# Kernel optimization log

Measured on AMD Instinct MI355X. Metric: run time of the kernel, lower is better.

Reference implementation:

```python
import jax, jax.numpy as jnp
import numpy as np

B_, T, I, S, O = 64, 2048, 64, 128, 64

def setup_inputs() -> dict:
    key = jax.random.key(0)
    ks = jax.random.split(key, 7)
    x = jax.random.normal(ks[0], (B_, T, I), dtype=jnp.float32)
    A = jax.random.normal(ks[1], (S, S), dtype=jnp.float32) * 0.1
    Bm = jax.random.normal(ks[2], (S, I), dtype=jnp.float32) * 0.1
    Cm = jax.random.normal(ks[3], (O, S), dtype=jnp.float32) * 0.1
    Dm = jax.random.normal(ks[4], (O, I), dtype=jnp.float32) * 0.1
    W_sel = jax.random.normal(ks[5], (S, I), dtype=jnp.float32) * 0.1
    b_sel = jnp.zeros((S,), jnp.float32)
    ln_gamma = jnp.ones((S,), jnp.float32)
    ln_beta = jnp.zeros((S,), jnp.float32)
    conv_w = jax.random.normal(ks[6], (S, I, 3), dtype=jnp.float32) * 0.1  # Conv1d weight [out,in,k]
    conv_b = jnp.zeros((S,), jnp.float32)
    return {"x": x, "A": A, "B": Bm, "C": Cm, "D": Dm, "W_sel": W_sel,
            "b_sel": b_sel, "ln_gamma": ln_gamma, "ln_beta": ln_beta,
            "conv_w": conv_w, "conv_b": conv_b, "use_parallel": 0}

LN_EPS = 1e-5

def _forward(x, A, B, C, D, W_sel, b_sel, ln_gamma, ln_beta, conv_w, conv_b, use_parallel):
    # x: [B, T, I]
    if use_parallel and x.shape[1] > 10:
        # parallel_scan: conv1d(k=3, pad=1) -> cumsum over time -> project with C
        xc = jnp.transpose(x, (0, 2, 1))  # [B, I, T]
        conv = jax.lax.conv_general_dilated(
            xc, conv_w, window_strides=(1,), padding=((1, 1),),
            dimension_numbers=("NCH", "OIH", "NCH")) + conv_b[None, :, None]
        conv = jnp.transpose(conv, (0, 2, 1))           # [B, T, S]
        out = jnp.cumsum(conv, axis=1) @ C.T            # [B, T, O]
    else:
        # selective_scan: sequential gated SSM with per-step LayerNorm
        def step(h, x_t):
            gate = jax.nn.sigmoid(x_t @ W_sel.T + b_sel)        # [B, S]
            h_new = h @ A.T + x_t @ B.T
            h = gate * h_new + (1.0 - gate) * h
            mu = jnp.mean(h, axis=-1, keepdims=True)
            var = jnp.var(h, axis=-1, keepdims=True)
            h = (h - mu) * jax.lax.rsqrt(var + LN_EPS) * ln_gamma + ln_beta
            y = h @ C.T + x_t @ D.T                              # [B, O]
            return h, y
        h0 = jnp.zeros((x.shape[0], A.shape[0]), x.dtype)
        _, ys = jax.lax.scan(step, h0, jnp.transpose(x, (1, 0, 2)))  # ys: [T, B, O]
        out = jnp.transpose(ys, (1, 0, 2))                           # [B, T, O]
    final = out[:, -1, :]
    diff = jnp.diff(out, axis=1)
    temporal_coherence = 1.0 / (1.0 + jnp.mean(jnp.linalg.norm(diff, axis=-1)))
    state_magnitude = jnp.mean(jnp.linalg.norm(out, axis=-1))
    selection_activity = jnp.mean(jax.nn.sigmoid(jnp.mean(x, axis=1) @ W_sel.T + b_sel))
    state_stability = jnp.mean(jnp.std(out, axis=1, ddof=1))  # torch.std is unbiased
    return final, temporal_coherence, state_magnitude, selection_activity, state_stability

def reference(x, A, B, C, D, W_sel, b_sel, ln_gamma, ln_beta, conv_w, conv_b, use_parallel):
    return _forward(x, A, B, C, D, W_sel, b_sel, ln_gamma, ln_beta, conv_w, conv_b, use_parallel)
```

## Files before the change

### kernel.cpp

```cpp
#include <hip/hip_runtime.h>
#include <math.h>

#define NB 64
#define NT 2048
#define NI 64
#define NS 128
#define NO 64

typedef float4 f4;

#define PIN4(v) asm("" : "+v"((v).x), "+v"((v).y), "+v"((v).z), "+v"((v).w))
#define FMA4(a0,a1,a2,a3,W_,V_) \
    a0 = fmaf((W_).x, (V_).x, a0); a1 = fmaf((W_).y, (V_).y, a1); \
    a2 = fmaf((W_).z, (V_).z, a2); a3 = fmaf((W_).w, (V_).w, a3)

template<int CTRL>
__device__ __forceinline__ float dpp_add(float v) {
    int t = __builtin_amdgcn_update_dpp(0, __float_as_int(v), CTRL, 0xF, 0xF, true);
    return v + __int_as_float(t);
}
__device__ __forceinline__ float qxor1(float v) { return dpp_add<0xB1>(v); }
__device__ __forceinline__ float qxor2(float v) { return dpp_add<0x4E>(v); }
__device__ __forceinline__ float wave_sum63(float v) {
    v = dpp_add<0x111>(v); v = dpp_add<0x112>(v); v = dpp_add<0x114>(v);
// ... 21 lines not shown
    const float* __restrict__ Wsel,
    const float* __restrict__ bsel,
    float* __restrict__ P)
{
    const int b   = blockIdx.x >> 5;
    const int c   = blockIdx.x & 31;
    const int tid = threadIdx.x;

    __shared__ __align__(16) float xs[64][64];
    {
        const f4* src = (const f4*)(x + ((size_t)b * NT + c * 64) * NI);
        f4* dst = (f4*)&xs[0][0];
        #pragma unroll
        for (int k = 0; k < 4; ++k) dst[tid + k * 256] = src[tid + k * 256];
    }

    const float* wrow = (tid < 128) ? (Bm + (size_t)tid * NI)
                                    : (Wsel + (size_t)(tid - 128) * NI);
    const float bias = (tid < 128) ? 0.f : bsel[tid - 128];

    f4 W0,W1,W2,W3,W4,W5,W6,W7,W8,W9,W10,W11,W12,W13,W14,W15;
    {
        const f4* wp = (const f4*)wrow;
        W0=wp[0]; W1=wp[1]; W2=wp[2]; W3=wp[3]; W4=wp[4]; W5=wp[5]; W6=wp[6]; W7=wp[7];
        W8=wp[8]; W9=wp[9]; W10=wp[10]; W11=wp[11]; W12=wp[12]; W13=wp[13]; W14=wp[14]; W15=wp[15];
    }
    PIN4(W0); PIN4(W1); PIN4(W2); PIN4(W3); PIN4(W4); PIN4(W5); PIN4(W6); PIN4(W7);
    PIN4(W8); PIN4(W9); PIN4(W10); PIN4(W11); PIN4(W12); PIN4(W13); PIN4(W14); PIN4(W15);

    __syncthreads();

// ... 11 lines not shown
        v = xr[6];  FMA4(a0,a1,a2,a3,W6,v);
        v = xr[7];  FMA4(a0,a1,a2,a3,W7,v);
        v = xr[8];  FMA4(a0,a1,a2,a3,W8,v);
        v = xr[9];  FMA4(a0,a1,a2,a3,W9,v);
        v = xr[10]; FMA4(a0,a1,a2,a3,W10,v);
        v = xr[11]; FMA4(a0,a1,a2,a3,W11,v);
        v = xr[12]; FMA4(a0,a1,a2,a3,W12,v);
        v = xr[13]; FMA4(a0,a1,a2,a3,W13,v);
        v = xr[14]; FMA4(a0,a1,a2,a3,W14,v);
        v = xr[15]; FMA4(a0,a1,a2,a3,W15,v);
        pout[(size_t)t * 256] = (a0 + a1) + (a2 + a3);
    }
}

template<int USEP>
__global__ __launch_bounds__(512, 2) void scan_kernel(
    const float* __restrict__ x,
    const float* __restrict__ P,
    const float* __restrict__ A,
    const float* __restrict__ Bm,
    const float* __restrict__ Wsel,
    const float* __restrict__ bsel,
    const float* __restrict__ gamma,
    const float* __restrict__ beta,
    float* __restrict__ H,
    float* __restrict__ musig)
{
    const int b    = blockIdx.x;
    const int tid  = threadIdx.x;
    const int q    = tid & 3;
    const int r    = tid >> 2;
    const int lane = tid & 63;
    const int wave = tid >> 6;

    __shared__ __align__(16) float hbuf[2][148];
    __shared__ __align__(16) float red[2][16];
    __shared__ __align__(16) float plds[2][32][USEP ? 256 : 64];

    f4 Aw0, Aw1, Aw2, Aw3, Aw4, Aw5, Aw6, Aw7;
    float sAg = 0.f, aB = 0.f;
    {
        const f4* ga = (const f4*)(gamma + q * 32);
        const f4* bb = (const f4*)(beta  + q * 32);
        const f4* Ap = (const f4*)(A + (size_t)r * NS + q * 32);
        f4 g, be_, v;
#define LOADA(J, AW) \
        g = ga[J]; be_ = bb[J]; v = Ap[J]; \
        AW.x = v.x * g.x; AW.y = v.y * g.y; AW.z = v.z * g.z; AW.w = v.w * g.w; \
        sAg += (AW.x + AW.y) + (AW.z + AW.w); \
        aB = fmaf(v.x, be_.x, aB); aB = fmaf(v.y, be_.y, aB); \
        aB = fmaf(v.z, be_.z, aB); aB = fmaf(v.w, be_.w, aB);
        LOADA(0, Aw0) LOADA(1, Aw1) LOADA(2, Aw2) LOADA(3, Aw3)
        LOADA(4, Aw4) LOADA(5, Aw5) LOADA(6, Aw6) LOADA(7, Aw7)
#undef LOADA
        sAg = qxor2(qxor1(sAg));
        aB  = qxor2(qxor1(aB));
    }
    PIN4(Aw0); PIN4(Aw1); PIN4(Aw2); PIN4(Aw3);
    PIN4(Aw4); PIN4(Aw5); PIN4(Aw6); PIN4(Aw7);

    f4 Bw0, Bw1, Bw2, Bw3, Ww0, Ww1, Ww2, Ww3;
    float bs = 0.f;
    if constexpr (!USEP) {
        const f4* Bp = (const f4*)(Bm   + (size_t)r * NI + q * 16);
        const f4* Wp = (const f4*)(Wsel + (size_t)r * NI + q * 16);
        Bw0 = Bp[0]; Bw1 = Bp[1]; Bw2 = Bp[2]; Bw3 = Bp[3];
        Ww0 = Wp[0]; Ww1 = Wp[1]; Ww2 = Wp[2]; Ww3 = Wp[3];
        bs = bsel[r];
        PIN4(Bw0); PIN4(Bw1); PIN4(Bw2); PIN4(Bw3);
        PIN4(Ww0); PIN4(Ww1); PIN4(Ww2); PIN4(Ww3);
        asm("" : "+v"(bs));
    }
    float gm = gamma[r], bt = beta[r];
    asm("" : "+v"(sAg), "+v"(aB), "+v"(gm), "+v"(bt));

    const float* xstage = x + (size_t)b * NT * NI + wave * 256 + lane * 4;
    const float* pstage = P + (size_t)b * NT * 256 + wave * 256 + lane * 4;
    if constexpr (USEP) {
        #pragma unroll
        for (int c = 0; c < 2; ++c)
            #pragma unroll
            for (int k = 0; k < 4; ++k)
                stage16(pstage + (size_t)(c * 32 + k * 8) * 256,
                        &plds[c][k * 8 + wave][0]);
    } else {
        stage16(xstage,        &plds[0][wave * 4][0]);
        stage16(xstage + 2048, &plds[1][wave * 4][0]);
    }
    asm volatile("s_waitcnt vmcnt(0)" ::: "memory");
    __syncthreads();

    float zp = 0.f, dBp = 0.f;
    float pbp = 0.f, pzp = 0.f;
    auto xdots = [&](int t) {
        const f4* xp = (const f4*)&plds[(t >> 5) & 1][t & 31][q * 16];
        f4 v0 = xp[0], v1 = xp[1], v2 = xp[2], v3 = xp[3];
        float p0 = 0.f, p1 = 0.f, p2 = 0.f, p3 = 0.f;
        float w0 = 0.f, w1 = 0.f, w2 = 0.f, w3 = 0.f;
        FMA4(p0, p1, p2, p3, Bw0, v0); FMA4(p0, p1, p2, p3, Bw1, v1);
        FMA4(p0, p1, p2, p3, Bw2, v2); FMA4(p0, p1, p2, p3, Bw3, v3);
        FMA4(w0, w1, w2, w3, Ww0, v0); FMA4(w0, w1, w2, w3, Ww1, v1);
        FMA4(w0, w1, w2, w3, Ww2, v2); FMA4(w0, w1, w2, w3, Ww3, v3);
        dBp = qxor2(qxor1((p0 + p1) + (p2 + p3)));
        zp  = qxor2(qxor1((w0 + w1) + (w2 + w3))) + bs;
    };
    auto pread = [&](int t) {
        const float* pl = &plds[(t >> 5) & 1][t & 31][0];
        pbp = pl[r]; pzp = pl[128 + r];
    };

    float*  Hb   = H + ((size_t)b * NT) * NS;
    float2* musb = (float2*)musig + (size_t)b * NT;

    float mp;
    if constexpr (USEP) pread(0); else xdots(0);
    {
        float g = sigmoidf_fast(USEP ? pzp : zp);
        mp = g * (USEP ? pbp : dBp);
        if (q == 0) {
            hbuf[0][((r >> 5) * 36) + (r & 31)] = mp;
            Hb[r] = mp;
        }
        float s  = wave_sum63(mp);
        float s2 = wave_sum63(mp * mp);
        if (lane == 63) { red[0][wave] = s; red[0][8 + wave] = s2; }
    }
    if constexpr (USEP) pread(1); else xdots(1);
    bar_lds();

    auto body = [&](int t, int parIn, int parOut) {
        const f4* rp = (const f4*)&red[parIn][0];
        f4 sa = rp[0], sb = rp[1], sc = rp[2], sd = rp[3];
        float S  = ((sa.x + sa.y) + (sa.z + sa.w)) + ((sb.x + sb.y) + (sb.z + sb.w));
        float S2 = ((sc.x + sc.y) + (sc.z + sc.w)) + ((sd.x + sd.y) + (sd.z + sd.w));
        float mu   = S * (1.0f / 512.0f);
        float var  = fmaf(S2, 1.0f / 512.0f, -mu * mu);
        float rstd = 1.0f / sqrtf(var + 1e-5f);
        const f4* hp = (const f4*)&hbuf[parIn][q * 36];
        f4 h0 = hp[0], h1 = hp[1], h2 = hp[2], h3 = hp[3];
        f4 h4 = hp[4], h5 = hp[5], h6 = hp[6], h7 = hp[7];
        float d0 = 0.f, d1 = 0.f, d2 = 0.f, d3 = 0.f;
        FMA4(d0, d1, d2, d3, Aw0, h0); FMA4(d0, d1, d2, d3, Aw1, h1);
        FMA4(d0, d1, d2, d3, Aw2, h2); FMA4(d0, d1, d2, d3, Aw3, h3);
        FMA4(d0, d1, d2, d3, Aw4, h4); FMA4(d0, d1, d2, d3, Aw5, h5);
        FMA4(d0, d1, d2, d3, Aw6, h6); FMA4(d0, d1, d2, d3, Aw7, h7);
        float dAm = qxor2(qxor1((d0 + d1) + (d2 + d3)));
        float dA  = fmaf(rstd, fmaf(-mu, sAg, dAm), aB);
        float hpl = fmaf((mp - mu) * rstd, gm, bt);
        float g   = sigmoidf_fast(USEP ? pzp : zp);
        float hn  = dA + (USEP ? pbp : dBp);
        float m   = fmaf(g, hn - hpl, hpl);
        if (q == 0) {
            hbuf[parOut][((r >> 5) * 36) + (r & 31)] = m;
            Hb[(size_t)t * NS + r] = m;
        }
        float s  = wave_sum63(m);
        float s2 = wave_sum63(m * m);
        if (lane == 63) { red[parOut][wave] = s; red[parOut][8 + wave] = s2; }
        if (tid == 0) musb[t - 1] = make_float2(mu, rstd);
        mp = m;
        if (t + 1 < NT) { if constexpr (USEP) pread(t + 1); else xdots(t + 1); }
        bar_lds();
    };

    auto boundary = [&](int t) {
        const int s2 = (t >> 5) + 2;
        if constexpr (USEP) {
            if (s2 < NT / 32) {
                #pragma unroll
                for (int k = 0; k < 4; ++k)
                    stage16(pstage + (size_t)(s2 * 32 + k * 8) * 256,
                            &plds[s2 & 1][k * 8 + wave][0]);
            }
            asm volatile("s_waitcnt vmcnt(4)" ::: "memory");
        } else {
            if (s2 < NT / 32)
                stage16(xstage + (size_t)s2 * 2048, &plds[s2 & 1][wave * 4][0]);
            asm volatile("s_waitcnt vmcnt(1)" ::: "memory");
        }
        __builtin_amdgcn_s_barrier();
        asm volatile("" ::: "memory");
    };

    for (int t = 1; t + 1 < NT; t += 2) {
        body(t, 0, 1);
        body(t + 1, 1, 0);
        if (((t + 1) & 31) == 30) boundary(t + 1);
    }
    body(NT - 1, 0, 1);

    {
        const f4* rp = (const f4*)&red[1][0];
        f4 sa = rp[0], sb = rp[1], sc = rp[2], sd = rp[3];
        float S  = ((sa.x + sa.y) + (sa.z + sa.w)) + ((sb.x + sb.y) + (sb.z + sb.w));
        float S2 = ((sc.x + sc.y) + (sc.z + sc.w)) + ((sd.x + sd.y) + (sd.z + sd.w));
        float mu   = S * (1.0f / 512.0f);
        float var  = fmaf(S2, 1.0f / 512.0f, -mu * mu);
        float rstd = 1.0f / sqrtf(var + 1e-5f);
        if (tid == 0) musb[NT - 1] = make_float2(mu, rstd);
    }
}

#define CHUNKS 32
#define TCH (NT / CHUNKS)

__global__ __launch_bounds__(512, 1) void y_stats_kernel(
    const float* __restrict__ H,
    const float* __restrict__ x,
    const float* __restrict__ Cm,
    const float* __restrict__ Dm,
    const float* __restrict__ gamma,
    const float* __restrict__ beta,
    const float* __restrict__ musig,
    float* __restrict__ SY,
    float* __restrict__ SYY,
    float* __restrict__ meanx,
    float* __restrict__ nsum,
    float* __restrict__ dsum,
    float* __restrict__ outFinal)
{
    const int b     = blockIdx.x >> 5;
    const int chunk = blockIdx.x & 31;
    const int tid   = threadIdx.x;
    const int o2    = tid & 31;
    const int kq    = (tid >> 5) & 3;
    const int tg    = tid >> 7;
    const int lane  = tid & 63;
    const int sub   = tid >> 6;
    const int o     = tid & 63;

    __shared__ float pbuf[TCH + 1][2 * NO];
    __shared__ float nd[2];

    f4 CA0,CA1,CA2,CA3,CA4,CA5,CA6,CA7, CB0,CB1,CB2,CB3,CB4,CB5,CB6,CB7;
    float sCgA = 0.f, cBA = 0.f, sCgB = 0.f, cBB = 0.f;
    {
        const f4* cpA = (const f4*)(Cm + (size_t)o2 * NS + kq * 32);
        const f4* cpB = (const f4*)(Cm + (size_t)(o2 + 32) * NS + kq * 32);
        const f4* gp  = (const f4*)(gamma + kq * 32);
        const f4* bp  = (const f4*)(beta  + kq * 32);
        f4 vv, gg, bb;
#define LC(J, CW, CP, SG, CBs) \
        vv = CP[J]; gg = gp[J]; bb = bp[J]; \
        CW.x = vv.x * gg.x; CW.y = vv.y * gg.y; CW.z = vv.z * gg.z; CW.w = vv.w * gg.w; \
        SG += (CW.x + CW.y) + (CW.z + CW.w); \
        CBs = fmaf(vv.x, bb.x, CBs); CBs = fmaf(vv.y, bb.y, CBs); \
        CBs = fmaf(vv.z, bb.z, CBs); CBs = fmaf(vv.w, bb.w, CBs);
        LC(0,CA0,cpA,sCgA,cBA) LC(1,CA1,cpA,sCgA,cBA) LC(2,CA2,cpA,sCgA,cBA) LC(3,CA3,cpA,sCgA,cBA)
        LC(4,CA4,cpA,sCgA,cBA) LC(5,CA5,cpA,sCgA,cBA) LC(6,CA6,cpA,sCgA,cBA) LC(7,CA7,cpA,sCgA,cBA)
        LC(0,CB0,cpB,sCgB,cBB) LC(1,CB1,cpB,sCgB,cBB) LC(2,CB2,cpB,sCgB,cBB) LC(3,CB3,cpB,sCgB,cBB)
        LC(4,CB4,cpB,sCgB,cBB) LC(5,CB5,cpB,sCgB,cBB) LC(6,CB6,cpB,sCgB,cBB) LC(7,CB7,cpB,sCgB,cBB)
#undef LC
    }
    f4 DA0,DA1,DA2,DA3, DB0,DB1,DB2,DB3;
    {
        const f4* dpA = (const f4*)(Dm + (size_t)o2 * NI + kq * 16);
        const f4* dpB = (const f4*)(Dm + (size_t)(o2 + 32) * NI + kq * 16);
        DA0 = dpA[0]; DA1 = dpA[1]; DA2 = dpA[2]; DA3 = dpA[3];
        DB0 = dpB[0]; DB1 = dpB[1]; DB2 = dpB[2]; DB3 = dpB[3];
    }
    PIN4(CA0); PIN4(CA1); PIN4(CA2); PIN4(CA3); PIN4(CA4); PIN4(CA5); PIN4(CA6); PIN4(CA7);
    PIN4(CB0); PIN4(CB1); PIN4(CB2); PIN4(CB3); PIN4(CB4); PIN4(CB5); PIN4(CB6); PIN4(CB7);
    PIN4(DA0); PIN4(DA1); PIN4(DA2); PIN4(DA3); PIN4(DB0); PIN4(DB1); PIN4(DB2); PIN4(DB3);
    asm("" : "+v"(sCgA), "+v"(cBA), "+v"(sCgB), "+v"(cBB));

    const float*  Hb  = H + ((size_t)b * NT) * NS;
    const float*  xb  = x + ((size_t)b * NT) * NI;
    const float2* msb = (const float2*)musig + (size_t)b * NT;
    const int t0 = chunk * TCH;

    if (tid < 2) nd[tid] = 0.f;

    if (sub < 4) {
        float s = 0.f;
        const float* xk = xb + o;
        #pragma unroll 4
        for (int i = 0; i < 16; ++i) s += xk[(size_t)(t0 + sub * 16 + i) * NI];
        atomicAdd(&meanx[b * NI + o], s);
    }

    {
        const int khigh = sub & 1;
        const int i_start = (tg == 0 && t0 > 0) ? -1 : 0;
        for (int i = i_start; i < 16; ++i) {
            const int t = t0 + tg * 16 + i;
            float2 ms = msb[t];
            const f4* hp = (const f4*)(Hb + (size_t)t * NS + kq * 32);
            const f4* xp = (const f4*)(xb + (size_t)t * NI + kq * 16);
            float a0=0.f,a1=0.f,a2=0.f,a3=0.f, b0=0.f,b1=0.f,b2=0.f,b3=0.f;
            f4 hv;
            hv = hp[0]; FMA4(a0,a1,a2,a3,CA0,hv); FMA4(b0,b1,b2,b3,CB0,hv);
            hv = hp[1]; FMA4(a0,a1,a2,a3,CA1,hv); FMA4(b0,b1,b2,b3,CB1,hv);
            hv = hp[2]; FMA4(a0,a1,a2,a3,CA2,hv); FMA4(b0,b1,b2,b3,CB2,hv);
            hv = hp[3]; FMA4(a0,a1,a2,a3,CA3,hv); FMA4(b0,b1,b2,b3,CB3,hv);
            hv = hp[4]; FMA4(a0,a1,a2,a3,CA4,hv); FMA4(b0,b1,b2,b3,CB4,hv);
            hv = hp[5]; FMA4(a0,a1,a2,a3,CA5,hv); FMA4(b0,b1,b2,b3,CB5,hv);
            hv = hp[6]; FMA4(a0,a1,a2,a3,CA6,hv); FMA4(b0,b1,b2,b3,CB6,hv);
            hv = hp[7]; FMA4(a0,a1,a2,a3,CA7,hv); FMA4(b0,b1,b2,b3,CB7,hv);
            float hdotA = (a0 + a1) + (a2 + a3);
            float hdotB = (b0 + b1) + (b2 + b3);
            float xa0=0.f,xa1=0.f,xa2=0.f,xa3=0.f, xb0=0.f,xb1=0.f,xb2=0.f,xb3=0.f;
            hv = xp[0]; FMA4(xa0,xa1,xa2,xa3,DA0,hv); FMA4(xb0,xb1,xb2,xb3,DB0,hv);
            hv = xp[1]; FMA4(xa0,xa1,xa2,xa3,DA1,hv); FMA4(xb0,xb1,xb2,xb3,DB1,hv);
            hv = xp[2]; FMA4(xa0,xa1,xa2,xa3,DA2,hv); FMA4(xb0,xb1,xb2,xb3,DB2,hv);
            hv = xp[3]; FMA4(xa0,xa1,xa2,xa3,DA3,hv); FMA4(xb0,xb1,xb2,xb3,DB3,hv);
            float xdotA = (xa0 + xa1) + (xa2 + xa3);
            float xdotB = (xb0 + xb1) + (xb2 + xb3);
            float pa = fmaf(ms.y, fmaf(-ms.x, sCgA, hdotA), cBA + xdotA);
            float pb = fmaf(ms.y, fmaf(-ms.x, sCgB, hdotB), cBB + xdotB);
            pa += __shfl_xor(pa, 32);
            pb += __shfl_xor(pb, 32);
            const int row = tg * 16 + i + 1;
            const int col = khigh * 64 + o2 + ((lane >= 32) ? 32 : 0);
            pbuf[row][col] = (lane >= 32) ? pb : pa;
        }
    }
    __syncthreads();

    {
        const int tt0 = sub * 8;
        float yprev = pbuf[tt0][o] + pbuf[tt0][64 + o];
        float sy = 0.f, syy = 0.f, na = 0.f, da = 0.f;
        #pragma unroll
        for (int ii = 0; ii < 8; ++ii) {
            const int row = tt0 + ii + 1;
            float y = pbuf[row][o] + pbuf[row][64 + o];
            sy  += y;
            syy += y * y;
            float n2 = wave_sum63(y * y);
            na += sqrtf(n2);
            if (t0 + tt0 + ii > 0) {
                float df = y - yprev;
                float d2 = wave_sum63(df * df);
                da += sqrtf(d2);
            }
            yprev = y;
            if (chunk == 31 && sub == 7 && ii == 7)
                outFinal[b * NO + o] = y;
        }
        atomicAdd(&SY[b * NO + o], sy);
        atomicAdd(&SYY[b * NO + o], syy);
        if (lane == 63) {
            atomicAdd(&nd[0], na);
            atomicAdd(&nd[1], da);
        }
    }
    __syncthreads();
    if (tid == 0) { atomicAdd(nsum, nd[0]); atomicAdd(dsum, nd[1]); }
}

__global__ __launch_bounds__(256) void finalize_kernel(
    const float* __restrict__ Wsel,
    const float* __restrict__ bsel,
    const float* __restrict__ meanx,
    const float* __restrict__ SY,
    const float* __restrict__ SYY,
    const float* __restrict__ nsum,
    const float* __restrict__ dsum,
    float* __restrict__ out)
{
    const int tid  = threadIdx.x;
    const int wave = tid >> 6;
    const int lane = tid & 63;
// ... 46 lines not shown
    const float* Bm    = (const float*)d_in[2];
    const float* Cm    = (const float*)d_in[3];
    const float* Dm    = (const float*)d_in[4];
    const float* Wsel  = (const float*)d_in[5];
    const float* bsel  = (const float*)d_in[6];
    const float* gamma = (const float*)d_in[7];
    const float* beta  = (const float*)d_in[8];
    float* out = (float*)d_out;

    char* ws = (char*)d_ws;
    float* SY    = (float*)(ws + 0);
    float* SYY   = (float*)(ws + 16384);
    float* meanx = (float*)(ws + 32768);
    float* nsum  = (float*)(ws + 49152);
    float* dsum  = (float*)(ws + 49156);
    const size_t zbytes = 49160;

    const size_t offH  = 65536;
    float* H     = (float*)(ws + offH);
    const size_t offMu = offH + (size_t)NB * NT * NS * sizeof(float);
    float* musig = (float*)(ws + offMu);
    const size_t offP  = offMu + (size_t)NB * NT * 2 * sizeof(float);
    float* P     = (float*)(ws + offP);
    const size_t needP = offP + (size_t)NB * NT * 256 * sizeof(float);

    const bool useP = (ws_size >= needP);

    hipMemsetAsync(ws, 0, zbytes, stream);
    if (useP) {
        proj_kernel<<<NB * 32, 256, 0, stream>>>(x, Bm, Wsel, bsel, P);
        scan_kernel<1><<<NB, 512, 0, stream>>>(x, P, A, Bm, Wsel, bsel,
                                               gamma, beta, H, musig);
    } else {
        scan_kernel<0><<<NB, 512, 0, stream>>>(x, (const float*)ws, A, Bm, Wsel,
                                               bsel, gamma, beta, H, musig);
    }
    y_stats_kernel<<<NB * CHUNKS, 512, 0, stream>>>(H, x, Cm, Dm, gamma, beta, musig,
                                                    SY, SYY, meanx, nsum, dsum, out);
    finalize_kernel<<<1, 256, 0, stream>>>(Wsel, bsel, meanx, SY, SYY, nsum, dsum, out);
}
```

Baseline: 1.681 ms.

## Fuse scan and output-stats kernels with producer-consumer progress flags

Merges the sequential scan kernel and the y-statistics kernel into one persistent launch. The first NB blocks run the per-batch scan and publish progress every 64 steps through release atomics. The remaining blocks act as consumers that spin on those flags and process 64-step chunks, so the output projection overlaps the scan instead of running after it. This relies on all blocks being co-resident and adds spin-wait and fence overhead, with fewer consumer blocks than the old separate grid.

Result: slower. 2.540 ms (+51.1%).

```diff
diff --git a/kernel.cpp b/kernel.cpp
--- a/kernel.cpp
+++ b/kernel.cpp
@@ -6,6 +6,8 @@
 #define NI 64
 #define NS 128
 #define NO 64
+
+#define LDS_BYTES 83968
 
 typedef float4 f4;
 
@@ -59,7 +61,6 @@
         #pragma unroll
         for (int k = 0; k < 4; ++k) dst[tid + k * 256] = src[tid + k * 256];
     }
-
     const float* wrow = (tid < 128) ? (Bm + (size_t)tid * NI)
                                     : (Wsel + (size_t)(tid - 128) * NI);
     const float bias = (tid < 128) ? 0.f : bsel[tid - 128];
@@ -101,7 +102,7 @@
 }
 
 template<int USEP>
-__global__ __launch_bounds__(512, 2) void scan_kernel(
+__global__ __launch_bounds__(512, 1) void fused_kernel(
     const float* __restrict__ x,
     const float* __restrict__ P,
     const float* __restrict__ A,
@@ -110,330 +111,350 @@
     const float* __restrict__ bsel,
     const float* __restrict__ gamma,
     const float* __restrict__ beta,
-    float* __restrict__ H,
-    float* __restrict__ musig)
-{
-    const int b    = blockIdx.x;
-    const int tid  = threadIdx.x;
-    const int q    = tid & 3;
-    const int r    = tid >> 2;
-    const int lane = tid & 63;
-    const int wave = tid >> 6;
-
-    __shared__ __align__(16) float hbuf[2][148];
-    __shared__ __align__(16) float red[2][16];
-    __shared__ __align__(16) float plds[2][32][USEP ? 256 : 64];
-
-    f4 Aw0, Aw1, Aw2, Aw3, Aw4, Aw5, Aw6, Aw7;
-    float sAg = 0.f, aB = 0.f;
-    {
-        const f4* ga = (const f4*)(gamma + q * 32);
-        const f4* bb = (const f4*)(beta  + q * 32);
-        const f4* Ap = (const f4*)(A + (size_t)r * NS + q * 32);
-        f4 g, be_, v;
-#define LOADA(J, AW) \
-        g = ga[J]; be_ = bb[J]; v = Ap[J]; \
-        AW.x = v.x * g.x; AW.y = v.y * g.y; AW.z = v.z * g.z; AW.w = v.w * g.w; \
-        sAg += (AW.x + AW.y) + (AW.z + AW.w); \
-        aB = fmaf(v.x, be_.x, aB); aB = fmaf(v.y, be_.y, aB); \
-        aB = fmaf(v.z, be_.z, aB); aB = fmaf(v.w, be_.w, aB);
-        LOADA(0, Aw0) LOADA(1, Aw1) LOADA(2, Aw2) LOADA(3, Aw3)
-        LOADA(4, Aw4) LOADA(5, Aw5) LOADA(6, Aw6) LOADA(7, Aw7)
-#undef LOADA
-        sAg = qxor2(qxor1(sAg));
-        aB  = qxor2(qxor1(aB));
-    }
-    PIN4(Aw0); PIN4(Aw1); PIN4(Aw2); PIN4(Aw3);
-    PIN4(Aw4); PIN4(Aw5); PIN4(Aw6); PIN4(Aw7);
-
-    f4 Bw0, Bw1, Bw2, Bw3, Ww0, Ww1, Ww2, Ww3;
-    float bs = 0.f;
-    if constexpr (!USEP) {
-        const f4* Bp = (const f4*)(Bm   + (size_t)r * NI + q * 16);
-        const f4* Wp = (const f4*)(Wsel + (size_t)r * NI + q * 16);
-        Bw0 = Bp[0]; Bw1 = Bp[1]; Bw2 = Bp[2]; Bw3 = Bp[3];
-        Ww0 = Wp[0]; Ww1 = Wp[1]; Ww2 = Wp[2]; Ww3 = Wp[3];
-        bs = bsel[r];
-        PIN4(Bw0); PIN4(Bw1); PIN4(Bw2); PIN4(Bw3);
-        PIN4(Ww0); PIN4(Ww1); PIN4(Ww2); PIN4(Ww3);
-        asm("" : "+v"(bs));
-    }
-    float gm = gamma[r], bt = beta[r];
-    asm("" : "+v"(sAg), "+v"(aB), "+v"(gm), "+v"(bt));
-
-    const float* xstage = x + (size_t)b * NT * NI + wave * 256 + lane * 4;
-    const float* pstage = P + (size_t)b * NT * 256 + wave * 256 + lane * 4;
-    if constexpr (USEP) {
-        #pragma unroll
-        for (int c = 0; c < 2; ++c)
-            #pragma unroll
-            for (int k = 0; k < 4; ++k)
-                stage16(pstage + (size_t)(c * 32 + k * 8) * 256,
-                        &plds[c][k * 8 + wave][0]);
-    } else {
-        stage16(xstage,        &plds[0][wave * 4][0]);
-        stage16(xstage + 2048, &plds[1][wave * 4][0]);
-    }
-    asm volatile("s_waitcnt vmcnt(0)" ::: "memory");
-    __syncthreads();
-
-    float zp = 0.f, dBp = 0.f;
-    float pbp = 0.f, pzp = 0.f;
-    auto xdots = [&](int t) {
-        const f4* xp = (const f4*)&plds[(t >> 5) & 1][t & 31][q * 16];
-        f4 v0 = xp[0], v1 = xp[1], v2 = xp[2], v3 = xp[3];
-        float p0 = 0.f, p1 = 0.f, p2 = 0.f, p3 = 0.f;
-        float w0 = 0.f, w1 = 0.f, w2 = 0.f, w3 = 0.f;
-        FMA4(p0, p1, p2, p3, Bw0, v0); FMA4(p0, p1, p2, p3, Bw1, v1);
-        FMA4(p0, p1, p2, p3, Bw2, v2); FMA4(p0, p1, p2, p3, Bw3, v3);
-        FMA4(w0, w1, w2, w3, Ww0, v0); FMA4(w0, w1, w2, w3, Ww1, v1);
-        FMA4(w0, w1, w2, w3, Ww2, v2); FMA4(w0, w1, w2, w3, Ww3, v3);
-        dBp = qxor2(qxor1((p0 + p1) + (p2 + p3)));
-        zp  = qxor2(qxor1((w0 + w1) + (w2 + w3))) + bs;
-    };
-    auto pread = [&](int t) {
-        const float* pl = &plds[(t >> 5) & 1][t & 31][0];
-        pbp = pl[r]; pzp = pl[128 + r];
-    };
-
-    float*  Hb   = H + ((size_t)b * NT) * NS;
-    float2* musb = (float2*)musig + (size_t)b * NT;
-
-    float mp;
-    if constexpr (USEP) pread(0); else xdots(0);
-    {
-        float g = sigmoidf_fast(USEP ? pzp : zp);
-        mp = g * (USEP ? pbp : dBp);
-        if (q == 0) {
-            hbuf[0][((r >> 5) * 36) + (r & 31)] = mp;
-            Hb[r] = mp;
-        }
-        float s  = wave_sum63(mp);
-        float s2 = wave_sum63(mp * mp);
-        if (lane == 63) { red[0][wave] = s; red[0][8 + wave] = s2; }
-    }
-    if constexpr (USEP) pread(1); else xdots(1);
-    bar_lds();
-
-    auto body = [&](int t, int parIn, int parOut) {
-        const f4* rp = (const f4*)&red[parIn][0];
-        f4 sa = rp[0], sb = rp[1], sc = rp[2], sd = rp[3];
-        float S  = ((sa.x + sa.y) + (sa.z + sa.w)) + ((sb.x + sb.y) + (sb.z + sb.w));
-        float S2 = ((sc.x + sc.y) + (sc.z + sc.w)) + ((sd.x + sd.y) + (sd.z + sd.w));
-        float mu   = S * (1.0f / 512.0f);
-        float var  = fmaf(S2, 1.0f / 512.0f, -mu * mu);
-        float rstd = 1.0f / sqrtf(var + 1e-5f);
-        const f4* hp = (const f4*)&hbuf[parIn][q * 36];
-        f4 h0 = hp[0], h1 = hp[1], h2 = hp[2], h3 = hp[3];
-        f4 h4 = hp[4], h5 = hp[5], h6 = hp[6], h7 = hp[7];
-        float d0 = 0.f, d1 = 0.f, d2 = 0.f, d3 = 0.f;
-        FMA4(d0, d1, d2, d3, Aw0, h0); FMA4(d0, d1, d2, d3, Aw1, h1);
-        FMA4(d0, d1, d2, d3, Aw2, h2); FMA4(d0, d1, d2, d3, Aw3, h3);
-        FMA4(d0, d1, d2, d3, Aw4, h4); FMA4(d0, d1, d2, d3, Aw5, h5);
-        FMA4(d0, d1, d2, d3, Aw6, h6); FMA4(d0, d1, d2, d3, Aw7, h7);
-        float dAm = qxor2(qxor1((d0 + d1) + (d2 + d3)));
-        float dA  = fmaf(rstd, fmaf(-mu, sAg, dAm), aB);
-        float hpl = fmaf((mp - mu) * rstd, gm, bt);
-        float g   = sigmoidf_fast(USEP ? pzp : zp);
-        float hn  = dA + (USEP ? pbp : dBp);
-        float m   = fmaf(g, hn - hpl, hpl);
-        if (q == 0) {
-            hbuf[parOut][((r >> 5) * 36) + (r & 31)] = m;
-            Hb[(size_t)t * NS + r] = m;
-        }
-        float s  = wave_sum63(m);
-        float s2 = wave_sum63(m * m);
-        if (lane == 63) { red[parOut][wave] = s; red[parOut][8 + wave] = s2; }
-        if (tid == 0) musb[t - 1] = make_float2(mu, rstd);
-        mp = m;
-        if (t + 1 < NT) { if constexpr (USEP) pread(t + 1); else xdots(t + 1); }
-        bar_lds();
-    };
-
-    auto boundary = [&](int t) {
-        const int s2 = (t >> 5) + 2;
-        if constexpr (USEP) {
-            if (s2 < NT / 32) {
-                #pragma unroll
-                for (int k = 0; k < 4; ++k)
-                    stage16(pstage + (size_t)(s2 * 32 + k * 8) * 256,
-                            &plds[s2 & 1][k * 8 + wave][0]);
-            }
-            asm volatile("s_waitcnt vmcnt(4)" ::: "memory");
-        } else {
-            if (s2 < NT / 32)
-                stage16(xstage + (size_t)s2 * 2048, &plds[s2 & 1][wave * 4][0]);
-            asm volatile("s_waitcnt vmcnt(1)" ::: "memory");
-        }
-        __builtin_amdgcn_s_barrier();
-        asm volatile("" ::: "memory");
-    };
-
-    for (int t = 1; t + 1 < NT; t += 2) {
-        body(t, 0, 1);
-        body(t + 1, 1, 0);
-        if (((t + 1) & 31) == 30) boundary(t + 1);
-    }
-    body(NT - 1, 0, 1);
-
-    {
-        const f4* rp = (const f4*)&red[1][0];
-        f4 sa = rp[0], sb = rp[1], sc = rp[2], sd = rp[3];
-        float S  = ((sa.x + sa.y) + (sa.z + sa.w)) + ((sb.x + sb.y) + (sb.z + sb.w));
-        float S2 = ((sc.x + sc.y) + (sc.z + sc.w)) + ((sd.x + sd.y) + (sd.z + sd.w));
-        float mu   = S * (1.0f / 512.0f);
-        float var  = fmaf(S2, 1.0f / 512.0f, -mu * mu);
-        float rstd = 1.0f / sqrtf(var + 1e-5f);
-        if (tid == 0) musb[NT - 1] = make_float2(mu, rstd);
-    }
-}
-
-#define CHUNKS 32
-#define TCH (NT / CHUNKS)
-
-__global__ __launch_bounds__(512, 1) void y_stats_kernel(
-    const float* __restrict__ H,
-    const float* __restrict__ x,
     const float* __restrict__ Cm,
     const float* __restrict__ Dm,
-    const float* __restrict__ gamma,
-    const float* __restrict__ beta,
-    const float* __restrict__ musig,
+    float* __restrict__ H,
+    float* __restrict__ musig,
     float* __restrict__ SY,
     float* __restrict__ SYY,
     float* __restrict__ meanx,
     float* __restrict__ nsum,
     float* __restrict__ dsum,
-    float* __restrict__ outFinal)
+    int*   __restrict__ progress,
+    float* __restrict__ outFinal,
+    int nCons)
 {
-    const int b     = blockIdx.x >> 5;
-    const int chunk = blockIdx.x & 31;
-    const int tid   = threadIdx.x;
-    const int o2    = tid & 31;
-    const int kq    = (tid >> 5) & 3;
-    const int tg    = tid >> 7;
-    const int lane  = tid & 63;
-    const int sub   = tid >> 6;
-    const int o     = tid & 63;
-
-    __shared__ float pbuf[TCH + 1][2 * NO];
-    __shared__ float nd[2];
-
-    f4 CA0,CA1,CA2,CA3,CA4,CA5,CA6,CA7, CB0,CB1,CB2,CB3,CB4,CB5,CB6,CB7;
-    float sCgA = 0.f, cBA = 0.f, sCgB = 0.f, cBB = 0.f;
+    __shared__ __align__(16) char raw[LDS_BYTES];
+    const int blk = blockIdx.x;
+    const int tid = threadIdx.x;
+    const int lane = tid & 63;
+    const int wave = tid >> 6;
+
+    if (blk < NB) {
+        const int b = blk;
+        const int q = tid & 3;
+        const int r = tid >> 2;
+        constexpr int PW = USEP ? 256 : 64;
+
+        float* hb   = (float*)raw;
+        float* rd   = (float*)(raw + 1184);
+        float* plds = (float*)(raw + 1312);
+
+        f4 Aw0, Aw1, Aw2, Aw3, Aw4, Aw5, Aw6, Aw7;
+        float sAg = 0.f, aB = 0.f;
+        {
+            const f4* ga = (const f4*)(gamma + q * 32);
+            const f4* bb = (const f4*)(beta  + q * 32);
+            const f4* Ap = (const f4*)(A + (size_t)r * NS + q * 32);
+            f4 g, be_, v;
+#define LOADA(J, AW) \
+            g = ga[J]; be_ = bb[J]; v = Ap[J]; \
+            AW.x = v.x * g.x; AW.y = v.y * g.y; AW.z = v.z * g.z; AW.w = v.w * g.w; \
+            sAg += (AW.x + AW.y) + (AW.z + AW.w); \
+            aB = fmaf(v.x, be_.x, aB); aB = fmaf(v.y, be_.y, aB); \
+            aB = fmaf(v.z, be_.z, aB); aB = fmaf(v.w, be_.w, aB);
+            LOADA(0, Aw0) LOADA(1, Aw1) LOADA(2, Aw2) LOADA(3, Aw3)
+            LOADA(4, Aw4) LOADA(5, Aw5) LOADA(6, Aw6) LOADA(7, Aw7)
+#undef LOADA
+            sAg = qxor2(qxor1(sAg));
+            aB  = qxor2(qxor1(aB));
+        }
+        PIN4(Aw0); PIN4(Aw1); PIN4(Aw2); PIN4(Aw3);
+        PIN4(Aw4); PIN4(Aw5); PIN4(Aw6); PIN4(Aw7);
+
+        f4 Bw0, Bw1, Bw2, Bw3, Ww0, Ww1, Ww2, Ww3;
+        float bs = 0.f;
+        if constexpr (!USEP) {
+            const f4* Bp = (const f4*)(Bm   + (size_t)r * NI + q * 16);
+            const f4* Wp = (const f4*)(Wsel + (size_t)r * NI + q * 16);
+            Bw0 = Bp[0]; Bw1 = Bp[1]; Bw2 = Bp[2]; Bw3 = Bp[3];
+            Ww0 = Wp[0]; Ww1 = Wp[1]; Ww2 = Wp[2]; Ww3 = Wp[3];
+            bs = bsel[r];
+            PIN4(Bw0); PIN4(Bw1); PIN4(Bw2); PIN4(Bw3);
+            PIN4(Ww0); PIN4(Ww1); PIN4(Ww2); PIN4(Ww3);
+            asm("" : "+v"(bs));
+        }
+        float gm = gamma[r], bt = beta[r];
+        asm("" : "+v"(sAg), "+v"(aB), "+v"(gm), "+v"(bt));
+
+        const float* xstage = x + (size_t)b * NT * NI + wave * 256 + lane * 4;
+        const float* pstage = P + (size_t)b * NT * 256 + wave * 256 + lane * 4;
+        if constexpr (USEP) {
+            #pragma unroll
+            for (int c = 0; c < 2; ++c)
+                #pragma unroll
+                for (int k = 0; k < 4; ++k)
+                    stage16(pstage + (size_t)(c * 32 + k * 8) * 256,
+                            plds + (c * 32 + k * 8 + wave) * PW);
+        } else {
+            stage16(xstage,        plds + (0 * 32 + wave * 4) * PW);
+            stage16(xstage + 2048, plds + (1 * 32 + wave * 4) * PW);
+        }
+        asm volatile("s_waitcnt vmcnt(0)" ::: "memory");
+        __syncthreads();
+
+        float zp = 0.f, dBp = 0.f, pbp = 0.f, pzp = 0.f;
+        auto xdots = [&](int t) {
+            const f4* xp = (const f4*)(plds + (((t >> 5) & 1) * 32 + (t & 31)) * PW + q * 16);
+            f4 v0 = xp[0], v1 = xp[1], v2 = xp[2], v3 = xp[3];
+            float p0 = 0.f, p1 = 0.f, p2 = 0.f, p3 = 0.f;
+            float w0 = 0.f, w1 = 0.f, w2 = 0.f, w3 = 0.f;
+            FMA4(p0, p1, p2, p3, Bw0, v0); FMA4(p0, p1, p2, p3, Bw1, v1);
+            FMA4(p0, p1, p2, p3, Bw2, v2); FMA4(p0, p1, p2, p3, Bw3, v3);
+            FMA4(w0, w1, w2, w3, Ww0, v0); FMA4(w0, w1, w2, w3, Ww1, v1);
+            FMA4(w0, w1, w2, w3, Ww2, v2); FMA4(w0, w1, w2, w3, Ww3, v3);
+            dBp = qxor2(qxor1((p0 + p1) + (p2 + p3)));
+            zp  = qxor2(qxor1((w0 + w1) + (w2 + w3))) + bs;
+        };
+        auto pread = [&](int t) {
+            const float* pl = plds + (((t >> 5) & 1) * 32 + (t & 31)) * PW;
+            pbp = pl[r]; pzp = pl[128 + r];
+        };
+
+        float*  Hb   = H + ((size_t)b * NT) * NS;
+        float2* musb = (float2*)musig + (size_t)b * NT;
+
+        float mp;
+        if constexpr (USEP) pread(0); else xdots(0);
+        {
+            float g = sigmoidf_fast(USEP ? pzp : zp);
+            mp = g * (USEP ? pbp : dBp);
+            if (q == 0) {
+                hb[0 * 148 + ((r >> 5) * 36) + (r & 31)] = mp;
+                Hb[r] = mp;
+            }
+            float s  = wave_sum63(mp);
+            float s2 = wave_sum63(mp * mp);
+            if (lane == 63) { rd[wave] = s; rd[8 + wave] = s2; }
+        }
+        if constexpr (USEP) pread(1); else xdots(1);
+        bar_lds();
+
+        auto body = [&](int t, int parIn, int parOut) {
+            const f4* rp = (const f4*)(rd + parIn * 16);
+            f4 sa = rp[0], sb = rp[1], sc = rp[2], sd = rp[3];
+            float S  = ((sa.x + sa.y) + (sa.z + sa.w)) + ((sb.x + sb.y) + (sb.z + sb.w));
+            float S2 = ((sc.x + sc.y) + (sc.z + sc.w)) + ((sd.x + sd.y) + (sd.z + sd.w));
+            float mu   = S * (1.0f / 512.0f);
+            float var  = fmaf(S2, 1.0f / 512.0f, -mu * mu);
+            float rstd = 1.0f / sqrtf(var + 1e-5f);
+            const f4* hp = (const f4*)(hb + parIn * 148 + q * 36);
+            f4 h0 = hp[0], h1 = hp[1], h2 = hp[2], h3 = hp[3];
+            f4 h4 = hp[4], h5 = hp[5], h6 = hp[6], h7 = hp[7];
+            float d0 = 0.f, d1 = 0.f, d2 = 0.f, d3 = 0.f;
+            FMA4(d0, d1, d2, d3, Aw0, h0); FMA4(d0, d1, d2, d3, Aw1, h1);
+            FMA4(d0, d1, d2, d3, Aw2, h2); FMA4(d0, d1, d2, d3, Aw3, h3);
+            FMA4(d0, d1, d2, d3, Aw4, h4); FMA4(d0, d1, d2, d3, Aw5, h5);
+            FMA4(d0, d1, d2, d3, Aw6, h6); FMA4(d0, d1, d2, d3, Aw7, h7);
+            float dAm = qxor2(qxor1((d0 + d1) + (d2 + d3)));
+            float dA  = fmaf(rstd, fmaf(-mu, sAg, dAm), aB);
+            float hpl = fmaf((mp - mu) * rstd, gm, bt);
+            float g   = sigmoidf_fast(USEP ? pzp : zp);
+            float hn  = dA + (USEP ? pbp : dBp);
+            float m   = fmaf(g, hn - hpl, hpl);
+            if (q == 0) {
+                hb[parOut * 148 + ((r >> 5) * 36) + (r & 31)] = m;
+                Hb[(size_t)t * NS + r] = m;
+            }
+            float s  = wave_sum63(m);
+            float s2 = wave_sum63(m * m);
+            if (lane == 63) { rd[parOut * 16 + wave] = s; rd[parOut * 16 + 8 + wave] = s2; }
+            if (tid == 0) musb[t - 1] = make_float2(mu, rstd);
+            mp = m;
+            if (t + 1 < NT) { if constexpr (USEP) pread(t + 1); else xdots(t + 1); }
+            bar_lds();
+        };
+
+        auto boundary = [&](int t) {
+            const int s2 = (t >> 5) + 2;
+            if constexpr (USEP) {
+                if (s2 < NT / 32) {
+                    #pragma unroll
+                    for (int k = 0; k < 4; ++k)
+                        stage16(pstage + (size_t)(s2 * 32 + k * 8) * 256,
+                                plds + ((s2 & 1) * 32 + k * 8 + wave) * PW);
+                }
+                asm volatile("s_waitcnt vmcnt(4)" ::: "memory");
+            } else {
+                if (s2 < NT / 32)
+                    stage16(xstage + (size_t)s2 * 2048, plds + ((s2 & 1) * 32 + wave * 4) * PW);
+                asm volatile("s_waitcnt vmcnt(1)" ::: "memory");
+            }
+            __builtin_amdgcn_s_barrier();
+            asm volatile("" ::: "memory");
+        };
+
+        for (int t = 1; t + 1 < NT; t += 2) {
+            body(t, 0, 1);
+            body(t + 1, 1, 0);
+            if (((t + 1) & 31) == 30) boundary(t + 1);
+            if (((t + 1) & 63) == 0) {
+                __threadfence();
+                __builtin_amdgcn_s_barrier();
+                if (tid == 0)
+                    __hip_atomic_store(&progress[b], (t + 1) >> 6,
+                                       __ATOMIC_RELEASE, __HIP_MEMORY_SCOPE_AGENT);
+            }
+        }
+        body(NT - 1, 0, 1);
+        {
+            const f4* rp = (const f4*)(rd + 1 * 16);
+            f4 sa = rp[0], sb = rp[1], sc = rp[2], sd = rp[3];
+            float S  = ((sa.x + sa.y) + (sa.z + sa.w)) + ((sb.x + sb.y) + (sb.z + sb.w));
+            float S2 = ((sc.x + sc.y) + (sc.z + sc.w)) + ((sd.x + sd.y) + (sd.z + sd.w));
+            float mu   = S * (1.0f / 512.0f);
+            float var  = fmaf(S2, 1.0f / 512.0f, -mu * mu);
+            float rstd = 1.0f / sqrtf(var + 1e-5f);
+            if (tid == 0) musb[NT - 1] = make_float2(mu, rstd);
+        }
+        __threadfence();
+        __builtin_amdgcn_s_barrier();
+        if (tid == 0)
+            __hip_atomic_store(&progress[b], 32,
+                               __ATOMIC_RELEASE, __HIP_MEMORY_SCOPE_AGENT);
+        return;
+    }
+
     {
-        const f4* cpA = (const f4*)(Cm + (size_t)o2 * NS + kq * 32);
-        const f4* cpB = (const f4*)(Cm + (size_t)(o2 + 32) * NS + kq * 32);
-        const f4* gp  = (const f4*)(gamma + kq * 32);
-        const f4* bp  = (const f4*)(beta  + kq * 32);
-        f4 vv, gg, bb;
+        const int k    = blk - NB;
+        const int o2   = tid & 31;
+        const int kq   = (tid >> 5) & 3;
+        const int tg   = tid >> 7;
+        const int sub  = tid >> 6;
+        const int o    = tid & 63;
+
+        float (*pbuf)[128] = (float(*)[128])raw;
+        float* nd = (float*)(raw + 65 * 128 * 4);
+
+        f4 CA0,CA1,CA2,CA3,CA4,CA5,CA6,CA7, CB0,CB1,CB2,CB3,CB4,CB5,CB6,CB7;
+        float sCgA = 0.f, cBA = 0.f, sCgB = 0.f, cBB = 0.f;
+        {
+            const f4* cpA = (const f4*)(Cm + (size_t)o2 * NS + kq * 32);
+            const f4* cpB = (const f4*)(Cm + (size_t)(o2 + 32) * NS + kq * 32);
+            const f4* gp  = (const f4*)(gamma + kq * 32);
+            const f4* bp  = (const f4*)(beta  + kq * 32);
+            f4 vv, gg, bb;
 #define LC(J, CW, CP, SG, CBs) \
-        vv = CP[J]; gg = gp[J]; bb = bp[J]; \
-        CW.x = vv.x * gg.x; CW.y = vv.y * gg.y; CW.z = vv.z * gg.z; CW.w = vv.w * gg.w; \
-        SG += (CW.x + CW.y) + (CW.z + CW.w); \
-        CBs = fmaf(vv.x, bb.x, CBs); CBs = fmaf(vv.y, bb.y, CBs); \
-        CBs = fmaf(vv.z, bb.z, CBs); CBs = fmaf(vv.w, bb.w, CBs);
-        LC(0,CA0,cpA,sCgA,cBA) LC(1,CA1,cpA,sCgA,cBA) LC(2,CA2,cpA,sCgA,cBA) LC(3,CA3,cpA,sCgA,cBA)
-        LC(4,CA4,cpA,sCgA,cBA) LC(5,CA5,cpA,sCgA,cBA) LC(6,CA6,cpA,sCgA,cBA) LC(7,CA7,cpA,sCgA,cBA)
-        LC(0,CB0,cpB,sCgB,cBB) LC(1,CB1,cpB,sCgB,cBB) LC(2,CB2,cpB,sCgB,cBB) LC(3,CB3,cpB,sCgB,cBB)
-        LC(4,CB4,cpB,sCgB,cBB) LC(5,CB5,cpB,sCgB,cBB) LC(6,CB6,cpB,sCgB,cBB) LC(7,CB7,cpB,sCgB,cBB)
+            vv = CP[J]; gg = gp[J]; bb = bp[J]; \
+            CW.x = vv.x * gg.x; CW.y = vv.y * gg.y; CW.z = vv.z * gg.z; CW.w = vv.w * gg.w; \
+            SG += (CW.x + CW.y) + (CW.z + CW.w); \
+            CBs = fmaf(vv.x, bb.x, CBs); CBs = fmaf(vv.y, bb.y, CBs); \
+            CBs = fmaf(vv.z, bb.z, CBs); CBs = fmaf(vv.w, bb.w, CBs);
+            LC(0,CA0,cpA,sCgA,cBA) LC(1,CA1,cpA,sCgA,cBA) LC(2,CA2,cpA,sCgA,cBA) LC(3,CA3,cpA,sCgA,cBA)
+            LC(4,CA4,cpA,sCgA,cBA) LC(5,CA5,cpA,sCgA,cBA) LC(6,CA6,cpA,sCgA,cBA) LC(7,CA7,cpA,sCgA,cBA)
+            LC(0,CB0,cpB,sCgB,cBB) LC(1,CB1,cpB,sCgB,cBB) LC(2,CB2,cpB,sCgB,cBB) LC(3,CB3,cpB,sCgB,cBB)
+            LC(4,CB4,cpB,sCgB,cBB) LC(5,CB5,cpB,sCgB,cBB) LC(6,CB6,cpB,sCgB,cBB) LC(7,CB7,cpB,sCgB,cBB)
 #undef LC
-    }
-    f4 DA0,DA1,DA2,DA3, DB0,DB1,DB2,DB3;
-    {
-        const f4* dpA = (const f4*)(Dm + (size_t)o2 * NI + kq * 16);
-        const f4* dpB = (const f4*)(Dm + (size_t)(o2 + 32) * NI + kq * 16);
-        DA0 = dpA[0]; DA1 = dpA[1]; DA2 = dpA[2]; DA3 = dpA[3];
-        DB0 = dpB[0]; DB1 = dpB[1]; DB2 = dpB[2]; DB3 = dpB[3];
-    }
-    PIN4(CA0); PIN4(CA1); PIN4(CA2); PIN4(CA3); PIN4(CA4); PIN4(CA5); PIN4(CA6); PIN4(CA7);
-    PIN4(CB0); PIN4(CB1); PIN4(CB2); PIN4(CB3); PIN4(CB4); PIN4(CB5); PIN4(CB6); PIN4(CB7);
-    PIN4(DA0); PIN4(DA1); PIN4(DA2); PIN4(DA3); PIN4(DB0); PIN4(DB1); PIN4(DB2); PIN4(DB3);
-    asm("" : "+v"(sCgA), "+v"(cBA), "+v"(sCgB), "+v"(cBB));
-
-    const float*  Hb  = H + ((size_t)b * NT) * NS;
-    const float*  xb  = x + ((size_t)b * NT) * NI;
-    const float2* msb = (const float2*)musig + (size_t)b * NT;
-    const int t0 = chunk * TCH;
-
-    if (tid < 2) nd[tid] = 0.f;
-
-    if (sub < 4) {
-        float s = 0.f;
-        const float* xk = xb + o;
-        #pragma unroll 4
-        for (int i = 0; i < 16; ++i) s += xk[(size_t)(t0 + sub * 16 + i) * NI];
-        atomicAdd(&meanx[b * NI + o], s);
-    }
-
-    {
-        const int khigh = sub & 1;
-        const int i_start = (tg == 0 && t0 > 0) ? -1 : 0;
-        for (int i = i_start; i < 16; ++i) {
-            const int t = t0 + tg * 16 + i;
-            float2 ms = msb[t];
-            const f4* hp = (const f4*)(Hb + (size_t)t * NS + kq * 32);
-            const f4* xp = (const f4*)(xb + (size_t)t * NI + kq * 16);
-            float a0=0.f,a1=0.f,a2=0.f,a3=0.f, b0=0.f,b1=0.f,b2=0.f,b3=0.f;
-            f4 hv;
-            hv = hp[0]; FMA4(a0,a1,a2,a3,CA0,hv); FMA4(b0,b1,b2,b3,CB0,hv);
-            hv = hp[1]; FMA4(a0,a1,a2,a3,CA1,hv); FMA4(b0,b1,b2,b3,CB1,hv);
-            hv = hp[2]; FMA4(a0,a1,a2,a3,CA2,hv); FMA4(b0,b1,b2,b3,CB2,hv);
-            hv = hp[3]; FMA4(a0,a1,a2,a3,CA3,hv); FMA4(b0,b1,b2,b3,CB3,hv);
-            hv = hp[4]; FMA4(a0,a1,a2,a3,CA4,hv); FMA4(b0,b1,b2,b3,CB4,hv);
-            hv = hp[5]; FMA4(a0,a1,a2,a3,CA5,hv); FMA4(b0,b1,b2,b3,CB5,hv);
-            hv = hp[6]; FMA4(a0,a1,a2,a3,CA6,hv); FMA4(b0,b1,b2,b3,CB6,hv);
-            hv = hp[7]; FMA4(a0,a1,a2,a3,CA7,hv); FMA4(b0,b1,b2,b3,CB7,hv);
-            float hdotA = (a0 + a1) + (a2 + a3);
-            float hdotB = (b0 + b1) + (b2 + b3);
-            float xa0=0.f,xa1=0.f,xa2=0.f,xa3=0.f, xb0=0.f,xb1=0.f,xb2=0.f,xb3=0.f;
-            hv = xp[0]; FMA4(xa0,xa1,xa2,xa3,DA0,hv); FMA4(xb0,xb1,xb2,xb3,DB0,hv);
-            hv = xp[1]; FMA4(xa0,xa1,xa2,xa3,DA1,hv); FMA4(xb0,xb1,xb2,xb3,DB1,hv);
-            hv = xp[2]; FMA4(xa0,xa1,xa2,xa3,DA2,hv); FMA4(xb0,xb1,xb2,xb3,DB2,hv);
-            hv = xp[3]; FMA4(xa0,xa1,xa2,xa3,DA3,hv); FMA4(xb0,xb1,xb2,xb3,DB3,hv);
-            float xdotA = (xa0 + xa1) + (xa2 + xa3);
-            float xdotB = (xb0 + xb1) + (xb2 + xb3);
-            float pa = fmaf(ms.y, fmaf(-ms.x, sCgA, hdotA), cBA + xdotA);
-            float pb = fmaf(ms.y, fmaf(-ms.x, sCgB, hdotB), cBB + xdotB);
-            pa += __shfl_xor(pa, 32);
-            pb += __shfl_xor(pb, 32);
-            const int row = tg * 16 + i + 1;
-            const int col = khigh * 64 + o2 + ((lane >= 32) ? 32 : 0);
-            pbuf[row][col] = (lane >= 32) ? pb : pa;
-        }
-    }
-    __syncthreads();
-
-    {
-        const int tt0 = sub * 8;
-        float yprev = pbuf[tt0][o] + pbuf[tt0][64 + o];
-        float sy = 0.f, syy = 0.f, na = 0.f, da = 0.f;
-        #pragma unroll
-        for (int ii = 0; ii < 8; ++ii) {
-            const int row = tt0 + ii + 1;
-            float y = pbuf[row][o] + pbuf[row][64 + o];
-            sy  += y;
-            syy += y * y;
-            float n2 = wave_sum63(y * y);
-            na += sqrtf(n2);
-            if (t0 + tt0 + ii > 0) {
-                float df = y - yprev;
-                float d2 = wave_sum63(df * df);
-                da += sqrtf(d2);
-            }
-            yprev = y;
-            if (chunk == 31 && sub == 7 && ii == 7)
-                outFinal[b * NO + o] = y;
-        }
-        atomicAdd(&SY[b * NO + o], sy);
-        atomicAdd(&SYY[b * NO + o], syy);
-        if (lane == 63) {
-            atomicAdd(&nd[0], na);
-            atomicAdd(&nd[1], da);
-        }
-    }
-    __syncthreads();
-    if (tid == 0) { atomicAdd(nsum, nd[0]); atomicAdd(dsum, nd[1]); }
+        }
+        f4 DA0,DA1,DA2,DA3, DB0,DB1,DB2,DB3;
+        {
+            const f4* dpA = (const f4*)(Dm + (size_t)o2 * NI + kq * 16);
+            const f4* dpB = (const f4*)(Dm + (size_t)(o2 + 32) * NI + kq * 16);
+            DA0 = dpA[0]; DA1 = dpA[1]; DA2 = dpA[2]; DA3 = dpA[3];
+            DB0 = dpB[0]; DB1 = dpB[1]; DB2 = dpB[2]; DB3 = dpB[3];
+        }
+        PIN4(CA0); PIN4(CA1); PIN4(CA2); PIN4(CA3); PIN4(CA4); PIN4(CA5); PIN4(CA6); PIN4(CA7);
+        PIN4(CB0); PIN4(CB1); PIN4(CB2); PIN4(CB3); PIN4(CB4); PIN4(CB5); PIN4(CB6); PIN4(CB7);
+        PIN4(DA0); PIN4(DA1); PIN4(DA2); PIN4(DA3); PIN4(DB0); PIN4(DB1); PIN4(DB2); PIN4(DB3);
+        asm("" : "+v"(sCgA), "+v"(cBA), "+v"(sCgB), "+v"(cBB));
+
+        if (tid < 2) nd[tid] = 0.f;
+        __syncthreads();
+
+        for (int u = k; u < NB * 32; u += nCons) {
+            const int c  = u >> 6;
+            const int bb = u & 63;
+            const float*  Hb  = H + ((size_t)bb * NT) * NS;
+            const float*  xb  = x + ((size_t)bb * NT) * NI;
+            const float2* msb = (const float2*)musig + (size_t)bb * NT;
+            const int t0 = c * 64;
+
+            if (sub < 4) {
+                float s = 0.f;
+                const float* xk = xb + o;
+                #pragma unroll 4
+                for (int i = 0; i < 16; ++i) s += xk[(size_t)(t0 + sub * 16 + i) * NI];
+                atomicAdd(&meanx[bb * NI + o], s);
+            }
+
+            if (tid == 0) {
+                while (__hip_atomic_load(&progress[bb], __ATOMIC_ACQUIRE,
+                                         __HIP_MEMORY_SCOPE_AGENT) <= c)
+                    __builtin_amdgcn_s_sleep(16);
+            }
+            __syncthreads();
+
+            {
+                const int khigh = sub & 1;
+                const int i_start = (tg == 0 && t0 > 0) ? -1 : 0;
+                for (int i = i_start; i < 16; ++i) {
+                    const int t = t0 + tg * 16 + i;
+                    float2 ms = msb[t];
+                    const f4* hp = (const f4*)(Hb + (size_t)t * NS + kq * 32);
+                    const f4* xp = (const f4*)(xb + (size_t)t * NI + kq * 16);
+                    float a0=0.f,a1=0.f,a2=0.f,a3=0.f, b0=0.f,b1=0.f,b2=0.f,b3=0.f;
+                    f4 hv;
+                    hv = hp[0]; FMA4(a0,a1,a2,a3,CA0,hv); FMA4(b0,b1,b2,b3,CB0,hv);
+                    hv = hp[1]; FMA4(a0,a1,a2,a3,CA1,hv); FMA4(b0,b1,b2,b3,CB1,hv);
+                    hv = hp[2]; FMA4(a0,a1,a2,a3,CA2,hv); FMA4(b0,b1,b2,b3,CB2,hv);
+                    hv = hp[3]; FMA4(a0,a1,a2,a3,CA3,hv); FMA4(b0,b1,b2,b3,CB3,hv);
+                    hv = hp[4]; FMA4(a0,a1,a2,a3,CA4,hv); FMA4(b0,b1,b2,b3,CB4,hv);
+                    hv = hp[5]; FMA4(a0,a1,a2,a3,CA5,hv); FMA4(b0,b1,b2,b3,CB5,hv);
+                    hv = hp[6]; FMA4(a0,a1,a2,a3,CA6,hv); FMA4(b0,b1,b2,b3,CB6,hv);
+                    hv = hp[7]; FMA4(a0,a1,a2,a3,CA7,hv); FMA4(b0,b1,b2,b3,CB7,hv);
+                    float hdotA = (a0 + a1) + (a2 + a3);
+                    float hdotB = (b0 + b1) + (b2 + b3);
+                    float xa0=0.f,xa1=0.f,xa2=0.f,xa3=0.f, xb0=0.f,xb1=0.f,xb2=0.f,xb3=0.f;
+                    hv = xp[0]; FMA4(xa0,xa1,xa2,xa3,DA0,hv); FMA4(xb0,xb1,xb2,xb3,DB0,hv);
+                    hv = xp[1]; FMA4(xa0,xa1,xa2,xa3,DA1,hv); FMA4(xb0,xb1,xb2,xb3,DB1,hv);
+                    hv = xp[2]; FMA4(xa0,xa1,xa2,xa3,DA2,hv); FMA4(xb0,xb1,xb2,xb3,DB2,hv);
+                    hv = xp[3]; FMA4(xa0,xa1,xa2,xa3,DA3,hv); FMA4(xb0,xb1,xb2,xb3,DB3,hv);
+                    float xdotA = (xa0 + xa1) + (xa2 + xa3);
+                    float xdotB = (xb0 + xb1) + (xb2 + xb3);
+                    float pa = fmaf(ms.y, fmaf(-ms.x, sCgA, hdotA), cBA + xdotA);
+                    float pb = fmaf(ms.y, fmaf(-ms.x, sCgB, hdotB), cBB + xdotB);
+                    pa += __shfl_xor(pa, 32);
+                    pb += __shfl_xor(pb, 32);
+                    const int row = tg * 16 + i + 1;
+                    const int col = khigh * 64 + o2 + ((lane >= 32) ? 32 : 0);
+                    pbuf[row][col] = (lane >= 32) ? pb : pa;
+                }
+            }
+            __syncthreads();
+
+            {
+                const int tt0 = sub * 8;
+                float yprev = pbuf[tt0][o] + pbuf[tt0][64 + o];
+                float sy = 0.f, syy = 0.f, na = 0.f, da = 0.f;
+                #pragma unroll
+                for (int ii = 0; ii < 8; ++ii) {
+                    const int row = tt0 + ii + 1;
+                    float y = pbuf[row][o] + pbuf[row][64 + o];
+                    sy  += y;
+                    syy += y * y;
+                    float n2 = wave_sum63(y * y);
+                    na += sqrtf(n2);
+                    if (t0 + tt0 + ii > 0) {
+                        float df = y - yprev;
+                        float d2 = wave_sum63(df * df);
+                        da += sqrtf(d2);
+                    }
+                    yprev = y;
+                    if (c == 31 && sub == 7 && ii == 7)
+                        outFinal[bb * NO + o] = y;
+                }
+                atomicAdd(&SY[bb * NO + o], sy);
+                atomicAdd(&SYY[bb * NO + o], syy);
+                if (lane == 63) {
+                    atomicAdd(&nd[0], na);
+                    atomicAdd(&nd[1], da);
+                }
+            }
+            __syncthreads();
+        }
+        __syncthreads();
+        if (tid == 0) { atomicAdd(nsum, nd[0]); atomicAdd(dsum, nd[1]); }
+    }
 }
 
 __global__ __launch_bounds__(256) void finalize_kernel(
@@ -510,7 +531,8 @@
     float* meanx = (float*)(ws + 32768);
     float* nsum  = (float*)(ws + 49152);
     float* dsum  = (float*)(ws + 49156);
-    const size_t zbytes = 49160;
+    int*   progress = (int*)(ws + 49160);
+    const size_t zbytes = 49160 + 256;
 
     const size_t offH  = 65536;
     float* H     = (float*)(ws + offH);
@@ -522,16 +544,23 @@
 
     const bool useP = (ws_size >= needP);
 
+    int dev = 0, mpc = 256;
+    hipGetDevice(&dev);
+    hipDeviceGetAttribute(&mpc, hipDeviceAttributeMultiprocessorCount, dev);
+    int grid = mpc < 256 ? mpc : 256;
+    if (grid < NB + 4) grid = NB + 4;
+    const int nCons = grid - NB;
+
     hipMemsetAsync(ws, 0, zbytes, stream);
     if (useP) {
         proj_kernel<<<NB * 32, 256, 0, stream>>>(x, Bm, Wsel, bsel, P);
-        scan_kernel<1><<<NB, 512, 0, stream>>>(x, P, A, Bm, Wsel, bsel,
-                                               gamma, beta, H, musig);
+        fused_kernel<1><<<grid, 512, 0, stream>>>(x, P, A, Bm, Wsel, bsel, gamma, beta,
+                                                  Cm, Dm, H, musig, SY, SYY, meanx,
+                                                  nsum, dsum, progress, out, nCons);
     } else {
-        scan_kernel<0><<<NB, 512, 0, stream>>>(x, (const float*)ws, A, Bm, Wsel,
-                                               bsel, gamma, beta, H, musig);
-    }
-    y_stats_kernel<<<NB * CHUNKS, 512, 0, stream>>>(H, x, Cm, Dm, gamma, beta, musig,
-                                                    SY, SYY, meanx, nsum, dsum, out);
+        fused_kernel<0><<<grid, 512, 0, stream>>>(x, (const float*)ws, A, Bm, Wsel, bsel,
+                                                  gamma, beta, Cm, Dm, H, musig, SY, SYY,
+                                                  meanx, nsum, dsum, progress, out, nCons);
+    }
     finalize_kernel<<<1, 256, 0, stream>>>(Wsel, bsel, meanx, SY, SYY, nsum, dsum, out);
 }
```
